# Performance work log

Measured on AMD Instinct MI355X. Metric: run time of the kernel, lower is better.

Reference implementation:

```python
import jax, jax.numpy as jnp
import numpy as np

LEAKY = 0.1
NSAMPLE = 16


def _gather_group(p, idx):
    # p: [B, N, C], idx: [B, S, K] -> [B, S, K, C]
    return jax.vmap(lambda pb, ib: pb[ib])(p, idx)


def _knn_idx(x, k):
    # x: [B, N, 3]; squared pairwise distances, smallest-k indices
    sq = jnp.sum(x * x, axis=-1)  # [B, N]
    d = sq[:, :, None] + sq[:, None, :] - 2.0 * jnp.einsum('bnc,bmc->bnm', x, x)
    _, idx = jax.lax.top_k(-d, k)  # [B, N, K]
    return idx


def setup_inputs() -> dict:
    key = jax.random.key(0)
    k1, k2, k3, k4, k5 = jax.random.split(key, 5)
    B, N, D = 4, 8192, 32
    m0, m1, m2 = 32, 32, 64
    xyz = jax.random.normal(k1, (B, 3, N), dtype=jnp.float32)
    points = jax.random.normal(k2, (B, D, N), dtype=jnp.float32)
    # Conv2d 1x1 weights (kernel dims squeezed): [out, in]
    W0 = jax.random.normal(k3, (m0, D + 3), dtype=jnp.float32) * (1.0 / np.sqrt(D + 3))
    W1 = jax.random.normal(k4, (m1, m0), dtype=jnp.float32) * (1.0 / np.sqrt(m0))
    W2 = jax.random.normal(k5, (m2, m1), dtype=jnp.float32) * (1.0 / np.sqrt(m1))
    return {'xyz': xyz, 'points': points, 'W0': W0, 'W1': W1, 'W2': W2}


def reference(xyz, points, W0, W1, W2):
    lrelu = lambda x: jax.nn.leaky_relu(x, LEAKY)
    xyz_t = jnp.swapaxes(xyz, 1, 2)  # [B, N, 3]
    # pre-transform point features with feature part of first conv weight
    feat = jnp.einsum('oc,bcn->bno', W0[:, 3:], points)  # [B, N, m0]
    idx = _knn_idx(xyz_t, NSAMPLE)  # [B, N, K]
    grouped_xyz = _gather_group(xyz_t, idx)              # [B, N, K, 3]
    grouped_norm = grouped_xyz - xyz_t[:, :, None, :]    # relative coords
    grouped_feat = _gather_group(feat, idx)              # [B, N, K, m0]
    # first conv: xyz-part applied to relative coords + already-transformed feats
    x = jnp.einsum('oc,bnkc->bonk', W0[:, :3], grouped_norm) \
        + jnp.transpose(grouped_feat, (0, 3, 1, 2))      # [B, m0, N, K]
    x = lrelu(x)
    x = lrelu(jnp.einsum('oc,bcnk->bonk', W1, x))        # [B, m1, N, K]
    x = lrelu(jnp.einsum('oc,bcnk->bonk', W2, x))        # [B, m2, N, K]
    return jnp.max(x, axis=-1)                           # [B, m2, N]
```

## Files before the change

kernel.cpp:

```cpp
#include <hip/hip_runtime.h>

#define NP   8192
#define BB   4
#define DIN  32
#define M0   32
#define M1   32
#define M2   64
#define CAP  80
#define CSTR 81
#define KQ   32

typedef float f32x2 __attribute__((ext_vector_type(2)));
typedef float f32x4 __attribute__((ext_vector_type(4)));
typedef short bf16x8 __attribute__((ext_vector_type(8)));

__device__ __forceinline__ float lrelu(float x) { return fmaxf(x, 0.1f * x); }
__device__ __forceinline__ unsigned umin_(unsigned a, unsigned b) { return a < b ? a : b; }
__device__ __forceinline__ unsigned umax_(unsigned a, unsigned b) { return a > b ? a : b; }

__device__ __forceinline__ unsigned fkey(float f) {
    unsigned b = __float_as_uint(f);
    return (b & 0x80000000u) ? ~b : (b | 0x80000000u);
}
__device__ __forceinline__ float funkey(unsigned k) {
    unsigned b = (k & 0x80000000u) ? (k & 0x7fffffffu) : ~k;
    return __uint_as_float(b);
}

__device__ __forceinline__ unsigned bf16rn(float f) {
    unsigned u = __float_as_uint(f);
    unsigned r = (u >> 16) & 1u;
    return (u + 0x7fffu + r) >> 16;
}

__device__ __forceinline__ f32x2 pk_fma(f32x2 a, f32x2 b, f32x2 c) {
    f32x2 d;
    asm("v_pk_fma_f32 %0, %1, %2, %3" : "=v"(d) : "v"(a), "s"(b), "v"(c));
    return d;
}

__device__ __forceinline__ void split_pack2(float f0, float f1, unsigned& hp, unsigned& lp) {
    unsigned u0 = __float_as_uint(f0), u1 = __float_as_uint(f1);
    unsigned h0 = u0 & 0xffff0000u, h1 = u1 & 0xffff0000u;
    hp = (u0 >> 16) | h1;
    float r0 = f0 - __uint_as_float(h0);
    float r1 = f1 - __uint_as_float(h1);
    lp = (__float_as_uint(r0) >> 16) | (__float_as_uint(r1) & 0xffff0000u);
}

__device__ __forceinline__ void wfrag(const float* wrow, bf16x8& h, bf16x8& lo) {
    float4 a = *(const float4*)(wrow);
    float4 b = *(const float4*)(wrow + 4);
    unsigned* hv = (unsigned*)&h;
    unsigned* lv = (unsigned*)&lo;
    split_pack2(a.x, a.y, hv[0], lv[0]);
    split_pack2(a.z, a.w, hv[1], lv[1]);
    split_pack2(b.x, b.y, hv[2], lv[2]);
    split_pack2(b.z, b.w, hv[3], lv[3]);
}

__device__ __forceinline__ f32x4 mfma16(bf16x8 a, bf16x8 b, f32x4 c) {
    return __builtin_amdgcn_mfma_f32_16x16x32_bf16(a, b, c, 0, 0, 0);
}

__global__ __launch_bounds__(256) void prep_kernel(
    const float* __restrict__ xyz, const float* __restrict__ points,
    const float* __restrict__ W0, const float* __restrict__ W1,
    const float* __restrict__ W2, float4* __restrict__ pts4,
    float4* __restrict__ ptsS, unsigned* __restrict__ featb,
    uint4* __restrict__ w1f, uint4* __restrict__ w2f)
{
    const int tid  = threadIdx.x;
    const int w    = __builtin_amdgcn_readfirstlane(tid >> 6);
    const int lane = tid & 63;
    const int t    = blockIdx.x * 64 + lane;
    const int b    = t >> 13;
    const int n    = t & (NP - 1);

    if (w == 0) {
        const float* xb = xyz + (size_t)b * 3 * NP;
        float x = xb[n], y = xb[NP + n], z = xb[2 * NP + n];
        float s = x * x + y * y + z * z;
        pts4[t] = make_float4(x, y, z, s);
        ptsS[t] = make_float4(-2.f * x, -2.f * y, -2.f * z, s);
    }

    const float* pb = points + (size_t)b * DIN * NP + n;
    float p[DIN];
#pragma unroll
    for (int c = 0; c < DIN; ++c) p[c] = pb[c * NP];

    uint4 outv;
    unsigned* ov = (unsigned*)&outv;
#pragma unroll
    for (int r = 0; r < 4; ++r) {
        int oe = w * 8 + 2 * r;
        float a0 = 0.f, a1 = 0.f;
#pragma unroll
        for (int c = 0; c < DIN; ++c) {
            a0 = fmaf(W0[oe * 35 + 3 + c], p[c], a0);
            a1 = fmaf(W0[(oe + 1) * 35 + 3 + c], p[c], a1);
        }
        ov[r] = bf16rn(a0) | (bf16rn(a1) << 16);
    }
    *(uint4*)(featb + (size_t)t * 16 + w * 4) = outv;

    if (blockIdx.x == 0 && tid < 64) {
        const int qq = tid & 15, gg = tid >> 4;
        bf16x8 h, lo;
#pragma unroll
        for (int r = 0; r < 2; ++r) {
            wfrag(W1 + (16 * r + qq) * 32 + gg * 8, h, lo);
            w1f[(r * 64 + tid) * 2 + 0] = *(uint4*)&h;
            w1f[(r * 64 + tid) * 2 + 1] = *(uint4*)&lo;
        }
#pragma unroll
        for (int rr = 0; rr < 4; ++rr) {
            wfrag(W2 + (16 * rr + qq) * 32 + gg * 8, h, lo);
            w2f[(rr * 64 + tid) * 2 + 0] = *(uint4*)&h;
            w2f[(rr * 64 + tid) * 2 + 1] = *(uint4*)&lo;
        }
    }
}

__global__ __launch_bounds__(512, 8) void knn_kernel(const float4* __restrict__ pts4,
                                                     const float4* __restrict__ ptsS,
                                                     int* __restrict__ idxout)
{
    __shared__ unsigned skey[KQ * 65];
    __shared__ float    sT[KQ];
    __shared__ int      scnt[KQ];
    __shared__ float    cand_t[KQ * CSTR];
    __shared__ int      cand_i[KQ * CSTR];

    const int tid  = threadIdx.x;
    const int w    = __builtin_amdgcn_readfirstlane(tid >> 6);
    const int lane = tid & 63;
    const int blk  = blockIdx.x;
    const int b    = blk >> 8;
    const int n0   = (blk & 255) << 5;
    const int bn0  = b * NP;
    const float4* P  = pts4 + bn0;
    const float4* S  = ptsS + bn0;
    const float4* Pq = P + n0;

    for (int i = tid; i < KQ * 65; i += 512) skey[i] = 0xFFFFFFFFu;
    if (tid < KQ) scnt[tid] = 0;
    __syncthreads();

    const int base = w * 1024;

#pragma unroll 1
    for (int sg = 0; sg < 2; ++sg) {
        const int sb = base + sg * 512;
        f32x2 sx[4], sy[4], sz[4], sw2[4];
#pragma unroll
        for (int jp = 0; jp < 4; ++jp) {
            float4 a = S[sb + (2 * jp) * 64 + lane];
            float4 c = S[sb + (2 * jp + 1) * 64 + lane];
            sx[jp].x = a.x;  sx[jp].y = c.x;
            sy[jp].x = a.y;  sy[jp].y = c.y;
            sz[jp].x = a.z;  sz[jp].y = c.z;
            sw2[jp].x = a.w; sw2[jp].y = c.w;
        }
#pragma unroll 1
        for (int qc = 0; qc < 4; ++qc) {
            float4 qv[8];
#pragma unroll
            for (int i = 0; i < 8; ++i) qv[i] = Pq[qc * 8 + i];
#pragma unroll
            for (int i = 0; i < 8; ++i) {
                f32x2 qx, qy, qz;
                qx.x = qv[i].x; qx.y = qv[i].x;
                qy.x = qv[i].y; qy.y = qv[i].y;
                qz.x = qv[i].z; qz.y = qv[i].z;
                f32x2 t0 = pk_fma(sz[0], qz, sw2[0]);
                f32x2 t1 = pk_fma(sz[1], qz, sw2[1]);
                f32x2 t2 = pk_fma(sz[2], qz, sw2[2]);
                f32x2 t3 = pk_fma(sz[3], qz, sw2[3]);
                t0 = pk_fma(sy[0], qy, t0);  t1 = pk_fma(sy[1], qy, t1);
                t2 = pk_fma(sy[2], qy, t2);  t3 = pk_fma(sy[3], qy, t3);
                t0 = pk_fma(sx[0], qx, t0);  t1 = pk_fma(sx[1], qx, t1);
                t2 = pk_fma(sx[2], qx, t2);  t3 = pk_fma(sx[3], qx, t3);
                float a  = fminf(fminf(t0.x, t0.y), t1.x);
                float b2 = fminf(fminf(t1.y, t2.x), t2.y);
                float c2 = fminf(fminf(t3.x, t3.y), a);
                float mn = fminf(b2, c2);
                atomicMin(&skey[(qc * 8 + i) * 65 + lane], fkey(mn));
            }
        }
    }
    __syncthreads();

#pragma unroll 1
    for (int qi = 0; qi < 4; ++qi) {
        const int q = w * 4 + qi;
        unsigned v = skey[q * 65 + lane];
#pragma unroll
        for (int k = 2; k <= 64; k <<= 1) {
#pragma unroll
            for (int j = k >> 1; j >= 1; j >>= 1) {
                unsigned o = __shfl_xor(v, j);
                bool lower = (lane & j) == 0;
                bool up    = (lane & k) == 0;
                unsigned mn = umin_(v, o), mx = umax_(v, o);
                v = (lower == up) ? mn : mx;
            }
        }
        if (lane == 15) sT[q] = funkey(v);
    }
    __syncthreads();

#pragma unroll 1
    for (int sg = 0; sg < 2; ++sg) {
        const int sb = base + sg * 512;
        f32x2 sx[4], sy[4], sz[4], sw2[4];
#pragma unroll
        for (int jp = 0; jp < 4; ++jp) {
            float4 a = S[sb + (2 * jp) * 64 + lane];
            float4 c = S[sb + (2 * jp + 1) * 64 + lane];
            sx[jp].x = a.x;  sx[jp].y = c.x;
            sy[jp].x = a.y;  sy[jp].y = c.y;
            sz[jp].x = a.z;  sz[jp].y = c.z;
            sw2[jp].x = a.w; sw2[jp].y = c.w;
        }
#pragma unroll 1
        for (int qc = 0; qc < 4; ++qc) {
            float4 qv[8];
#pragma unroll
            for (int i = 0; i < 8; ++i) qv[i] = Pq[qc * 8 + i];
#pragma unroll
            for (int i = 0; i < 8; ++i) {
                const int q = qc * 8 + i;
                const float T = sT[q];
                f32x2 qx, qy, qz;
                qx.x = qv[i].x; qx.y = qv[i].x;
                qy.x = qv[i].y; qy.y = qv[i].y;
                qz.x = qv[i].z; qz.y = qv[i].z;
#pragma unroll
                for (int jp = 0; jp < 4; ++jp) {
                    f32x2 t = pk_fma(sz[jp], qz, sw2[jp]);
                    t = pk_fma(sy[jp], qy, t);
                    t = pk_fma(sx[jp], qx, t);
                    if (t.x <= T) {
                        int pos = atomicAdd(&scnt[q], 1);
                        if (pos < CAP) {
                            cand_t[q * CSTR + pos] = t.x;
                            cand_i[q * CSTR + pos] = sb + (2 * jp) * 64 + lane;
                        }
                    }
                    if (t.y <= T) {
                        int pos = atomicAdd(&scnt[q], 1);
                        if (pos < CAP) {
                            cand_t[q * CSTR + pos] = t.y;
                            cand_i[q * CSTR + pos] = sb + (2 * jp + 1) * 64 + lane;
                        }
                    }
                }
            }
        }
    }
    __syncthreads();

#pragma unroll 1
    for (int qi = 0; qi < 4; ++qi) {
        const int q = w * 4 + qi;
        const int cnt = scnt[q];
        int* outp = idxout + ((bn0 + n0 + q) << 4);
        if (cnt <= CAP) {
            unsigned kh = 0xFFFFFFFFu, kl = 0xFFFFFFFFu;
            if (lane < cnt) {
                kh = fkey(cand_t[q * CSTR + lane]);
                kl = (unsigned)cand_i[q * CSTR + lane];
            }
#pragma unroll
            for (int k = 2; k <= 64; k <<= 1) {
#pragma unroll
                for (int j = k >> 1; j >= 1; j >>= 1) {
                    unsigned oh = __shfl_xor(kh, j);
                    unsigned ol = __shfl_xor(kl, j);
                    bool lower = (lane & j) == 0;
                    bool up    = (lane & k) == 0;
                    bool lt    = (kh < oh) || (kh == oh && kl < ol);
                    bool keep  = ((lower == up) == lt);
                    kh = keep ? kh : oh;
                    kl = keep ? kl : ol;
                }
            }
            for (int e = 64; e < cnt; ++e) {
                unsigned eh = fkey(cand_t[q * CSTR + e]);
                unsigned el = (unsigned)cand_i[q * CSTR + e];
                unsigned long long less = __ballot((kh < eh) || (kh == eh && kl < el));
                int r = (int)__popcll(less);
                unsigned ph = __shfl_up(kh, 1);
                unsigned pl = __shfl_up(kl, 1);
                if (lane == r)      { kh = eh; kl = el; }
                else if (lane > r)  { kh = ph; kl = pl; }
            }
            if (lane < 16) outp[lane] = (int)kl;
        } else if (lane == 0) {
            float bd[16]; int bi[16];
#pragma unroll
            for (int i = 0; i < 16; ++i) { bd[i] = 3e38f; bi[i] = 0; }
            float4 q4 = Pq[q];
            for (int j = 0; j < NP; ++j) {
                float4 s = S[j];
                float d = fmaf(q4.x, s.x, fmaf(q4.y, s.y, fmaf(q4.z, s.z, s.w)));
                if ((d < bd[15]) || (d == bd[15] && j < bi[15])) {
                    bd[15] = d; bi[15] = j;
#pragma unroll
                    for (int i = 15; i > 0; --i) {
                        bool sw = (bd[i] < bd[i - 1]) || (bd[i] == bd[i - 1] && bi[i] < bi[i - 1]);
                        float td = bd[i - 1]; int tj = bi[i - 1];
                        bd[i - 1] = sw ? bd[i] : td;  bi[i - 1] = sw ? bi[i] : tj;
                        bd[i]     = sw ? td : bd[i];  bi[i]     = sw ? tj : bi[i];
                    }
                }
            }
#pragma unroll
            for (int i = 0; i < 16; ++i) outp[i] = bi[i];
        }
    }
}

__global__ __launch_bounds__(256, 4) void conv_kernel(
    const float4* __restrict__ pts4, const unsigned* __restrict__ featb,
    const int* __restrict__ idx, const float* __restrict__ W0,
    const uint4* __restrict__ w1f, const uint4* __restrict__ w2f,
    float* __restrict__ out)
{
    __shared__ __align__(16) unsigned short sh_hi[4][4][64][8];
    __shared__ __align__(16) unsigned short sh_lo[4][4][64][8];
    float* soF = (float*)&sh_lo[0][0][0][0];

    const int tid = threadIdx.x;
    const int w   = __builtin_amdgcn_readfirstlane(tid >> 6);
    const int l   = tid & 63;
    const int g   = l >> 4;
    const int q   = l & 15;
    const int k   = tid & 15;
    const int nl  = tid >> 4;
    const int blk = blockIdx.x;
    const int b   = blk >> 9;
    const int n0  = (blk & 511) << 4;
    const int n   = n0 + nl;
    const int bn  = b * NP + n;
    const int j   = idx[(bn << 4) + k];
    const int bj  = b * NP + j;

    const float4 pc = pts4[bn];
    const float4 pj = pts4[bj];
    const float rx = pj.x - pc.x, ry = pj.y - pc.y, rz = pj.z - pc.z;

    const uint4* fj = (const uint4*)(featb + (size_t)bj * 16);

#pragma unroll
    for (int gg = 0; gg < 4; ++gg) {
        uint4 u = fj[gg];
        const unsigned* uv = (const unsigned*)&u;
        uint4 hv, lv;
        unsigned* hp = (unsigned*)&hv;
        unsigned* lp = (unsigned*)&lv;
#pragma unroll
        for (int r = 0; r < 4; ++r) {
            int o = gg * 8 + 2 * r;
            float fe  = __uint_as_float(uv[r] << 16);
            float fo_ = __uint_as_float(uv[r] & 0xffff0000u);
            float e0 = lrelu(fmaf(W0[o * 35], rx, fmaf(W0[o * 35 + 1], ry, fmaf(W0[o * 35 + 2], rz, fe))));
            float e1 = lrelu(fmaf(W0[(o + 1) * 35], rx, fmaf(W0[(o + 1) * 35 + 1], ry, fmaf(W0[(o + 1) * 35 + 2], rz, fo_))));
            split_pack2(e0, e1, hp[r], lp[r]);
        }
        *(uint4*)&sh_hi[w][gg][l][0] = hv;
        *(uint4*)&sh_lo[w][gg][l][0] = lv;
    }

    bf16x8 b1h[4], b1l[4];
#pragma unroll
    for (int t = 0; t < 4; ++t) {
        b1h[t] = *(const bf16x8*)&sh_hi[w][g][16 * t + q][0];
        b1l[t] = *(const bf16x8*)&sh_lo[w][g][16 * t + q][0];
    }
    const f32x4 zz = {0.f, 0.f, 0.f, 0.f};
#pragma unroll
    for (int r = 0; r < 2; ++r) {
        bf16x8 wh = *(const bf16x8*)&w1f[(r * 64 + l) * 2 + 0];
        bf16x8 wl = *(const bf16x8*)&w1f[(r * 64 + l) * 2 + 1];
#pragma unroll
        for (int t = 0; t < 4; ++t) {
            f32x4 a = mfma16(wl, b1h[t], zz);
            a = mfma16(wh, b1l[t], a);
            a = mfma16(wh, b1h[t], a);
            float v0 = lrelu(a[0]);
            float v1 = lrelu(a[1]);
            float v2 = lrelu(a[2]);
            float v3 = lrelu(a[3]);
            uint2 hv, lv;
            split_pack2(v0, v1, hv.x, lv.x);
            split_pack2(v2, v3, hv.y, lv.y);
            const int kg = 2 * r + (g >> 1);
            const int ko = 4 * (g & 1);
            *(uint2*)&sh_hi[w][kg][16 * t + q][ko] = hv;
            *(uint2*)&sh_lo[w][kg][16 * t + q][ko] = lv;
        }
    }

    bf16x8 b2h[4], b2l[4];
#pragma unroll
    for (int t = 0; t < 4; ++t) {
        b2h[t] = *(const bf16x8*)&sh_hi[w][g][16 * t + q][0];
        b2l[t] = *(const bf16x8*)&sh_lo[w][g][16 * t + q][0];
    }
    __syncthreads();

#pragma unroll
    for (int rr = 0; rr < 4; ++rr) {
        bf16x8 wh = *(const bf16x8*)&w2f[(rr * 64 + l) * 2 + 0];
        bf16x8 wl = *(const bf16x8*)&w2f[(rr * 64 + l) * 2 + 1];
#pragma unroll
        for (int t = 0; t < 4; ++t) {
            f32x4 a = mfma16(b2h[t], wl, zz);
            a = mfma16(b2l[t], wh, a);
            a = mfma16(b2h[t], wh, a);
            float m = fmaxf(fmaxf(a[0], a[1]), fmaxf(a[2], a[3]));
            m = fmaxf(m, __int_as_float(__builtin_amdgcn_ds_swizzle(__float_as_int(m), 0x401F)));
            m = fmaxf(m, __shfl_xor(m, 32));
            if (g == 0) soF[(16 * rr + q) * 17 + w * 4 + t] = lrelu(m);
        }
    }
    __syncthreads();
    {
        int o = tid >> 2;
        int col = (tid & 3) << 2;
        float4 v = make_float4(soF[o * 17 + col], soF[o * 17 + col + 1],
                               soF[o * 17 + col + 2], soF[o * 17 + col + 3]);
        *(float4*)(out + ((size_t)(b * M2 + o)) * NP + n0 + col) = v;
    }
}

extern "C" void kernel_launch(void* const* d_in, const int* in_sizes, int n_in,
                              void* d_out, int out_size, void* d_ws, size_t ws_size,
                              hipStream_t stream)
{
    const float* xyz    = (const float*)d_in[0];
    const float* points = (const float*)d_in[1];
    const float* W0     = (const float*)d_in[2];
    const float* W1     = (const float*)d_in[3];
    const float* W2     = (const float*)d_in[4];
    float* out = (float*)d_out;

    char* ws = (char*)d_ws;
    float4*   pts4  = (float4*)ws;
    float4*   ptsS  = (float4*)(ws + 0x080000);
    unsigned* featb = (unsigned*)(ws + 0x100000);
    int*      idx   = (int*)(ws + 0x300000);
    uint4*    w1f   = (uint4*)(ws + 0x500000);
    uint4*    w2f   = (uint4*)(ws + 0x502000);

    prep_kernel<<<BB * NP / 64, 256,  0, stream>>>(xyz, points, W0, W1, W2, pts4, ptsS, featb, w1f, w2f);
    knn_kernel <<<BB * NP / KQ, 512,  0, stream>>>(pts4, ptsS, idx);
    conv_kernel<<<BB * NP / 16, 256,  0, stream>>>(pts4, featb, idx, W0, w1f, w2f, out);
}
```

Measured before the change: 172.7 us.

## Shrink KNN blocks to 16 queries, aggregate candidate atomics per wave, use hardware bf16 packing

Result: slower. 183.3 us (+6.2%).

```diff
diff --git a/kernel.cpp b/kernel.cpp
--- a/kernel.cpp
+++ b/kernel.cpp
@@ -8,7 +8,7 @@
 #define M2   64
 #define CAP  80
 #define CSTR 81
-#define KQ   32
+#define KQ   16
 
 typedef float f32x2 __attribute__((ext_vector_type(2)));
 typedef float f32x4 __attribute__((ext_vector_type(4)));
@@ -46,6 +46,17 @@
     float r0 = f0 - __uint_as_float(h0);
     float r1 = f1 - __uint_as_float(h1);
     lp = (__float_as_uint(r0) >> 16) | (__float_as_uint(r1) & 0xffff0000u);
+}
+
+__device__ __forceinline__ void split_pack_fast(float f0, float f1, unsigned& hp, unsigned& lp) {
+    unsigned u0 = __float_as_uint(f0), u1 = __float_as_uint(f1);
+    unsigned h0 = u0 & 0xffff0000u, h1 = u1 & 0xffff0000u;
+    hp = (u0 >> 16) | h1;
+    float r0 = f0 - __uint_as_float(h0);
+    float r1 = f1 - __uint_as_float(h1);
+    unsigned lo;
+    asm("v_cvt_pk_bf16_f32 %0, %1, %2" : "=v"(lo) : "v"(r0), "v"(r1));
+    lp = lo;
 }
 
 __device__ __forceinline__ void wfrag(const float* wrow, bf16x8& h, bf16x8& lo) {
@@ -123,7 +134,7 @@
     }
 }
 
-__global__ __launch_bounds__(512, 8) void knn_kernel(const float4* __restrict__ pts4,
+__global__ __launch_bounds__(256, 8) void knn_kernel(const float4* __restrict__ pts4,
                                                      const float4* __restrict__ ptsS,
                                                      int* __restrict__ idxout)
 {
@@ -137,21 +148,21 @@
     const int w    = __builtin_amdgcn_readfirstlane(tid >> 6);
     const int lane = tid & 63;
     const int blk  = blockIdx.x;
-    const int b    = blk >> 8;
-    const int n0   = (blk & 255) << 5;
+    const int b    = blk >> 9;
+    const int n0   = (blk & 511) << 4;
     const int bn0  = b * NP;
     const float4* P  = pts4 + bn0;
     const float4* S  = ptsS + bn0;
     const float4* Pq = P + n0;
 
-    for (int i = tid; i < KQ * 65; i += 512) skey[i] = 0xFFFFFFFFu;
+    for (int i = tid; i < KQ * 65; i += 256) skey[i] = 0xFFFFFFFFu;
     if (tid < KQ) scnt[tid] = 0;
     __syncthreads();
 
-    const int base = w * 1024;
-
-#pragma unroll 1
-    for (int sg = 0; sg < 2; ++sg) {
+    const int base = w * 2048;
+
+#pragma unroll 1
+    for (int sg = 0; sg < 4; ++sg) {
         const int sb = base + sg * 512;
         f32x2 sx[4], sy[4], sz[4], sw2[4];
 #pragma unroll
@@ -164,7 +175,7 @@
             sw2[jp].x = a.w; sw2[jp].y = c.w;
         }
 #pragma unroll 1
-        for (int qc = 0; qc < 4; ++qc) {
+        for (int qc = 0; qc < 2; ++qc) {
             float4 qv[8];
 #pragma unroll
             for (int i = 0; i < 8; ++i) qv[i] = Pq[qc * 8 + i];
@@ -212,7 +223,7 @@
     __syncthreads();
 
 #pragma unroll 1
-    for (int sg = 0; sg < 2; ++sg) {
+    for (int sg = 0; sg < 4; ++sg) {
         const int sb = base + sg * 512;
         f32x2 sx[4], sy[4], sz[4], sw2[4];
 #pragma unroll
@@ -225,7 +236,7 @@
             sw2[jp].x = a.w; sw2[jp].y = c.w;
         }
 #pragma unroll 1
-        for (int qc = 0; qc < 4; ++qc) {
+        for (int qc = 0; qc < 2; ++qc) {
             float4 qv[8];
 #pragma unroll
             for (int i = 0; i < 8; ++i) qv[i] = Pq[qc * 8 + i];
@@ -242,18 +253,28 @@
                     f32x2 t = pk_fma(sz[jp], qz, sw2[jp]);
                     t = pk_fma(sy[jp], qy, t);
                     t = pk_fma(sx[jp], qx, t);
-                    if (t.x <= T) {
-                        int pos = atomicAdd(&scnt[q], 1);
-                        if (pos < CAP) {
-                            cand_t[q * CSTR + pos] = t.x;
-                            cand_i[q * CSTR + pos] = sb + (2 * jp) * 64 + lane;
+                    bool c0 = (t.x <= T), c1 = (t.y <= T);
+                    unsigned long long m0 = __ballot(c0);
+                    unsigned long long m1 = __ballot(c1);
+                    if (m0 | m1) {
+                        int ntot = (int)__popcll(m0) + (int)__popcll(m1);
+                        int basep = 0;
+                        if (lane == 0) basep = atomicAdd(&scnt[q], ntot);
+                        basep = __shfl(basep, 0);
+                        unsigned long long below = (1ull << lane) - 1ull;
+                        if (c0) {
+                            int pos = basep + (int)__popcll(m0 & below);
+                            if (pos < CAP) {
+                                cand_t[q * CSTR + pos] = t.x;
+                                cand_i[q * CSTR + pos] = sb + (2 * jp) * 64 + lane;
+                            }
                         }
-                    }
-                    if (t.y <= T) {
-                        int pos = atomicAdd(&scnt[q], 1);
-                        if (pos < CAP) {
-                            cand_t[q * CSTR + pos] = t.y;
-                            cand_i[q * CSTR + pos] = sb + (2 * jp + 1) * 64 + lane;
+                        if (c1) {
+                            int pos = basep + (int)__popcll(m0) + (int)__popcll(m1 & below);
+                            if (pos < CAP) {
+                                cand_t[q * CSTR + pos] = t.y;
+                                cand_i[q * CSTR + pos] = sb + (2 * jp + 1) * 64 + lane;
+                            }
                         }
                     }
                 }
@@ -368,7 +389,7 @@
             float fo_ = __uint_as_float(uv[r] & 0xffff0000u);
             float e0 = lrelu(fmaf(W0[o * 35], rx, fmaf(W0[o * 35 + 1], ry, fmaf(W0[o * 35 + 2], rz, fe))));
             float e1 = lrelu(fmaf(W0[(o + 1) * 35], rx, fmaf(W0[(o + 1) * 35 + 1], ry, fmaf(W0[(o + 1) * 35 + 2], rz, fo_))));
-            split_pack2(e0, e1, hp[r], lp[r]);
+            split_pack_fast(e0, e1, hp[r], lp[r]);
         }
         *(uint4*)&sh_hi[w][gg][l][0] = hv;
         *(uint4*)&sh_lo[w][gg][l][0] = lv;
@@ -395,8 +416,8 @@
             float v2 = lrelu(a[2]);
             float v3 = lrelu(a[3]);
             uint2 hv, lv;
-            split_pack2(v0, v1, hv.x, lv.x);
-            split_pack2(v2, v3, hv.y, lv.y);
+            split_pack_fast(v0, v1, hv.x, lv.x);
+            split_pack_fast(v2, v3, hv.y, lv.y);
             const int kg = 2 * r + (g >> 1);
             const int ko = 4 * (g & 1);
             *(uint2*)&sh_hi[w][kg][16 * t + q][ko] = hv;
@@ -457,6 +478,6 @@
     uint4*    w2f   = (uint4*)(ws + 0x502000);
 
     prep_kernel<<<BB * NP / 64, 256,  0, stream>>>(xyz, points, W0, W1, W2, pts4, ptsS, featb, w1f, w2f);
-    knn_kernel <<<BB * NP / KQ, 512,  0, stream>>>(pts4, ptsS, idx);
+    knn_kernel <<<BB * NP / KQ, 256,  0, stream>>>(pts4, ptsS, idx);
     conv_kernel<<<BB * NP / 16, 256,  0, stream>>>(pts4, featb, idx, W0, w1f, w2f, out);
 }
```
